# Optimization experiments

Measured on AMD Instinct MI355X. Metric: run time of the kernel, lower is better.

The kernel has to match this reference:

```python
import jax, jax.numpy as jnp
import numpy as np

K = 8            # hard-coded knn k
NS = 0.2         # LeakyReLU negative slope
EPS = 1e-6
LN_EPS = 1e-5
H = 6            # num_heads


def vn_lin(W, x):
    # VNLinear: linear over vector-channel dim (axis 1). x: (B, Cin, 3, ...)
    return jnp.einsum('oc,bc...->bo...', W, x)


def vn_leaky(x, W, U):
    # VNLinearLeakyReLU (no BN): feature map p, direction map d
    p = vn_lin(W, x)
    d = vn_lin(U, x)
    dot = jnp.sum(p * d, axis=2, keepdims=True)
    dsq = jnp.sum(d * d, axis=2, keepdims=True)
    neg = p - (dot / (dsq + EPS)) * d
    return NS * p + (1.0 - NS) * jnp.where(dot >= 0, p, neg)


def vn_layernorm(x, g, b):
    # LayerNorm on per-channel vector norms, rescale directions. x: (B,C,3,N)
    n = jnp.sqrt(jnp.sum(x * x, axis=2) + EPS)            # (B,C,N)
    mu = jnp.mean(n, axis=1, keepdims=True)
    var = jnp.var(n, axis=1, keepdims=True)
    nhat = (n - mu) / jnp.sqrt(var + LN_EPS)
    nnew = g[None, :, None] * nhat + b[None, :, None]
    return x * (nnew / n)[:, :, None, :]


def vn_attention(vn_x, Wq, Wk, Wv, Wo):
    # vn_x: (B, C, 3, N); VNLinear(C, 3C) projections, multi-head SDPA over N
    B, C, _, N = vn_x.shape
    def heads(W):
        t = vn_lin(W, vn_x)                               # (B, 3C, 3, N)
        t = t.reshape(B, H, 3 * C // H, 3, N)
        return t.transpose(0, 1, 4, 2, 3).reshape(B, H, N, -1)  # (B,H,N,9C/H)
    q, k, v = heads(Wq), heads(Wk), heads(Wv)
    scale = (3 * C // H) ** -0.5                          # head_dim = dim//H = 64
    attn = jax.nn.softmax(jnp.einsum('bhqd,bhkd->bhqk', q, k) * scale, axis=-1)
    o = jnp.einsum('bhqk,bhkd->bhqd', attn, v)            # (B,H,N,9C/H)
    o = o.transpose(0, 2, 1, 3).reshape(B, N, 3 * C, 3).transpose(0, 2, 3, 1)
    return vn_lin(Wo, o)                                  # (B, C, 3, N)


def vn_get_graph_feature(x, knn_index):
    # x: (B, C, 3, N); knn_index: flat (B*K*N,) into (B*N) rows
    B, C, _, N = x.shape
    xp = x.transpose(0, 3, 1, 2).reshape(B * N, C * 3)
    feat = xp[knn_index].reshape(B, K, N, C, 3)
    xc = x.transpose(0, 3, 1, 2).reshape(B, 1, N, C, 3)
    f = jnp.concatenate([feat - xc, jnp.broadcast_to(xc, (B, K, N, C, 3))], axis=3)
    return f.transpose(0, 3, 4, 2, 1)                     # (B, 2C, 3, N, K)


def setup_inputs() -> dict:
    key = jax.random.key(0)
    ks = jax.random.split(key, 20)
    B, N, C = 4, 2048, 128
    def w(k, o, i):
        return jax.random.normal(k, (o, i), jnp.float32) * (i ** -0.5)
    return {
        'x': jax.random.normal(ks[0], (B, N, 3 * C), jnp.float32),
        'knn_index': jax.random.randint(ks[1], (B * K * N,), 0, B * N),
        'g1': jnp.ones((C,), jnp.float32), 'b1': jnp.zeros((C,), jnp.float32),
        'g2': jnp.ones((C,), jnp.float32), 'b2': jnp.zeros((C,), jnp.float32),
        'Wq': w(ks[2], 3 * C, C), 'Wk': w(ks[3], 3 * C, C), 'Wv': w(ks[4], 3 * C, C),
        'Wo': w(ks[5], C, 3 * C),
        'W1': w(ks[6], C, 2 * C), 'U1': w(ks[7], C, 2 * C),   # conv1: 256->128
        'W2': w(ks[8], C, 2 * C),                               # conv2: 256->128
        'W3': w(ks[9], 2 * C, C), 'U3': w(ks[10], 2 * C, C),   # conv3: 128->256
        'W4': w(ks[11], C, 2 * C), 'U4': w(ks[12], C, 2 * C),  # conv4: 256->128
    }


def reference(x, knn_index, g1, b1, g2, b2, Wq, Wk, Wv, Wo, W1, U1, W2, W3, U3, W4, U4):
    B, N, D = x.shape
    C = D // 3
    vn_x = x.transpose(0, 2, 1).reshape(B, C, 3, N)
    norm_x = vn_layernorm(vn_x, g1, b1)
    x_1 = vn_attention(norm_x, Wq, Wk, Wv, Wo)            # (B,C,3,N)
    knn_f = vn_get_graph_feature(norm_x, knn_index)       # (B,2C,3,N,K)
    knn_f = vn_leaky(knn_f, W1, U1)                       # (B,C,3,N,K)
    knn_f = jnp.mean(knn_f, axis=-1)                      # mean_pool over k
    x_1 = jnp.concatenate([x_1, knn_f], axis=1)           # (B,2C,3,N)
    x_1 = vn_lin(W2, x_1)                                 # (B,C,3,N)
    vn_x = vn_x + x_1
    nx2 = vn_layernorm(vn_x, g2, b2)
    h = vn_leaky(nx2, W3, U3)                             # (B,2C,3,N)
    h = vn_leaky(h, W4, U4)                               # (B,C,3,N)
    vn_x = vn_x + h
    return vn_x.reshape(B, D, N).transpose(0, 2, 1)       # (B,N,384)
```

## Files before the change

### kernel.cpp

```cpp
#include <hip/hip_runtime.h>
#include <math.h>

#define NFIX 2048
#define HH 6
#define KNN 8
#define NSLOPE 0.2f
#define EPSF 1e-6f
#define LNEPSF 1e-5f
#define QSCALE 0.18033688011112042f
#define NSPLIT 2

typedef unsigned short ushort_t;
typedef unsigned int uint_t;
typedef __attribute__((ext_vector_type(8))) short bf16x8;
typedef __attribute__((ext_vector_type(4))) short bf16x4;
typedef __attribute__((ext_vector_type(8))) _Float16 f16x8;
typedef __attribute__((ext_vector_type(4))) _Float16 f16x4;
typedef __attribute__((ext_vector_type(16))) float f32x16;
typedef __attribute__((ext_vector_type(4))) float f32x4;

__device__ __forceinline__ ushort_t f2bf(float f) {
  union { float f; unsigned u; } v; v.f = f;
  unsigned r = v.u + 0x7fff + ((v.u >> 16) & 1);
  return (ushort_t)(r >> 16);
}
__device__ __forceinline__ float bf2f(ushort_t u) {
  union { uint_t u; float f; } v; v.u = ((uint_t)u) << 16; return v.f;
}
__device__ __forceinline__ uint_t pack2(float a, float b) {
  return (uint_t)f2bf(a) | ((uint_t)f2bf(b) << 16);
}
__device__ __forceinline__ ushort_t f2h_bits(float a) {
  union { _Float16 h; ushort_t s; } cv; cv.h = (_Float16)a; return cv.s;
}
__device__ __forceinline__ uint_t packh2(float a, float b) {
  union { _Float16 h; ushort_t s; } ha, hb;
  ha.h = (_Float16)a; hb.h = (_Float16)b;
  return (uint_t)ha.s | ((uint_t)hb.s << 16);
}

__device__ __forceinline__ void vnleaky3(const float* p, const float* dv, float* out) {
  float dot = p[0]*dv[0] + p[1]*dv[1] + p[2]*dv[2];
  float dsq = dv[0]*dv[0] + dv[1]*dv[1] + dv[2]*dv[2] + EPSF;
  float f = dot / dsq;
#pragma unroll
  for (int d = 0; d < 3; ++d) {
    float neg = p[d] - f * dv[d];
    out[d] = NSLOPE * p[d] + (1.f - NSLOPE) * ((dot >= 0.f) ? p[d] : neg);
  }
}

__global__ __launch_bounds__(256) void prep_ln1(
    const float* __restrict__ Wq, const float* __restrict__ Wk,
    const float* __restrict__ Wv, const float* __restrict__ Wo,
    const float* __restrict__ W1, const float* __restrict__ U1,
    const float* __restrict__ W2, const float* __restrict__ W3,
    const float* __restrict__ U3, const float* __restrict__ W4,
    const float* __restrict__ U4,
    ushort_t* __restrict__ Wall, _Float16* __restrict__ Af16,
    _Float16* __restrict__ W3h, _Float16* __restrict__ U3h,
    _Float16* __restrict__ W4h, _Float16* __restrict__ U4h,
    const float* __restrict__ xin, ushort_t* __restrict__ xbp,
    float* __restrict__ xdi, const float* __restrict__ g1,
    const float* __restrict__ b1) {
  __shared__ float red[8];
  int bi = blockIdx.x;
  if (bi >= 1600) {
    int t = threadIdx.x;
    int half = t >> 7, c = t & 127;
    int bn = (bi - 1600) * 2 + half;
    const float* row = xin + (size_t)bn * 384;
    float x0 = row[c*3+0], x1 = row[c*3+1], x2 = row[c*3+2];
    float nv = sqrtf(x0*x0 + x1*x1 + x2*x2 + EPSF);
    float s1 = nv, s2 = nv*nv;
#pragma unroll
    for (int off = 32; off >= 1; off >>= 1) {
      s1 += __shfl_down(s1, off);
      s2 += __shfl_down(s2, off);
    }
    int lane = t & 63, w = t >> 6;
    if (lane == 0) { red[w*2] = s1; red[w*2+1] = s2; }
    __syncthreads();
    int rb4 = (w >> 1) * 4;
    float tot1 = red[rb4] + red[rb4+2], tot2 = red[rb4+1] + red[rb4+3];
    float mu  = tot1 * (1.f/128.f);
    float var = tot2 * (1.f/128.f) - mu*mu;
    float rsig = rsqrtf(var + LNEPSF);
    float nnew = g1[c] * ((nv - mu) * rsig) + b1[c];
    float sc = nnew / nv;
    size_t rb = (size_t)bn * 384;
    xbp[rb + c]       = f2bf(x0*sc);
    xbp[rb + 128 + c] = f2bf(x1*sc);
    xbp[rb + 256 + c] = f2bf(x2*sc);
    xdi[rb + c]       = x0;
    xdi[rb + 128 + c] = x1;
    xdi[rb + 256 + c] = x2;
    return;
  }
  int idx = bi * 256 + threadIdx.x;
  if (idx < 212992) {
    int m = idx >> 7, c = idx & 127;
    float val;
    if (m < 384)       val = Wq[m*128 + c] * QSCALE;
    else if (m < 768)  val = Wk[(m-384)*128 + c];
    else if (m < 1152) val = Wv[(m-768)*128 + c];
    else {
      int j = m - 1152;
      if (j < 128)      val = W1[j*256 + c];
      else if (j < 256) val = U1[(j-128)*256 + c];
      else if (j < 384) { int o = j-256; val = W1[o*256 + 128 + c] - W1[o*256 + c]; }
      else              { int o = j-384; val = U1[o*256 + 128 + c] - U1[o*256 + c]; }
    }
    Wall[idx] = f2bf(val); return;
  }
  idx -= 212992;
  if (idx < 49152) {
    int c = idx / 384, j = idx % 384;
    float s = 0.f;
    for (int cp = 0; cp < 128; ++cp) s += W2[c*256 + cp] * Wo[cp*384 + j];
    Af16[(size_t)c*512 + j] = (_Float16)s; return;
  }
  idx -= 49152;
  if (idx < 16384) {
    int c2 = idx / 128, c = idx % 128;
    Af16[(size_t)c*512 + 384 + c2] = (_Float16)W2[c*256 + 128 + c2]; return;
  }
  idx -= 16384;
  if (idx < 32768) { W3h[idx] = (_Float16)W3[idx]; return; }
  idx -= 32768;
  if (idx < 32768) { U3h[idx] = (_Float16)U3[idx]; return; }
  idx -= 32768;
  if (idx < 32768) { W4h[idx] = (_Float16)W4[idx]; return; }
  idx -= 32768;
  if (idx < 32768) { U4h[idx] = (_Float16)U4[idx]; return; }
}

#define XT_PITCH 132
#define WT_PITCH 132
#define TR_PITCH 36
__global__ __launch_bounds__(256, 2) void qkv_conv1_mfma(
    const ushort_t* __restrict__ xb, const ushort_t* __restrict__ Wall,
    ushort_t* __restrict__ q, ushort_t* __restrict__ k, ushort_t* __restrict__ v,
    _Float16* __restrict__ YZh, _Float16* __restrict__ NBh) {
  __shared__ ushort_t xs[128*XT_PITCH];
  __shared__ ushort_t wt[2][32*WT_PITCH];
  __shared__ float tr[4][32*TR_PITCH];
  int nb = blockIdx.x % 192;
  int mq = blockIdx.x / 192;
  int n0 = nb * 128;
  int t = threadIdx.x;
  int w = t >> 6, lane = t & 63, ql = lane & 31, hl = lane >> 5;
  for (int idx = t; idx < 2048; idx += 256) {
    int n = idx >> 4, c16 = idx & 15;
    bf16x8 gv = *(const bf16x8*)&xb[(size_t)(n0 + n)*128 + c16*8];
    ushort_t* dst = &xs[n*XT_PITCH + c16*8];
    *(bf16x4*)dst = __builtin_shufflevector(gv, gv, 0, 1, 2, 3);
    *(bf16x4*)(dst+4) = __builtin_shufflevector(gv, gv, 4, 5, 6, 7);
  }
#pragma unroll
  for (int i = 0; i < 2; ++i) {
    int idx = i*256 + t;
    int mm = idx >> 4, c16 = idx & 15;
    bf16x8 gv = *(const bf16x8*)&Wall[(size_t)(mq*416 + mm)*128 + c16*8];
    ushort_t* dst = &wt[0][mm*WT_PITCH + c16*8];
    *(bf16x4*)dst = __builtin_shufflevector(gv, gv, 0, 1, 2, 3);
    *(bf16x4*)(dst+4) = __builtin_shufflevector(gv, gv, 4, 5, 6, 7);
  }
  __syncthreads();
  bf16x8 xf[8];
  {
    const ushort_t* xr = &xs[(w*32 + ql)*XT_PITCH + hl*8];
#pragma unroll
    for (int cs = 0; cs < 8; ++cs) {
      bf16x4 lo = *(const bf16x4*)(xr + cs*16);
      bf16x4 hi = *(const bf16x4*)(xr + cs*16 + 4);
      xf[cs] = __builtin_shufflevector(lo, hi, 0, 1, 2, 3, 4, 5, 6, 7);
    }
  }
  int ng = n0 + w*32 + ql;
  int pt = ng / 3;
  int d  = ng - 3*pt;
  float* trw = tr[w];
  int mm0 = t >> 4, c160 = t & 15;
  int mm1 = (t + 256) >> 4, c161 = t & 15;
  for (int mt = 0; mt < 13; ++mt) {
    int m0 = mq*416 + mt*32;
    int cur = mt & 1;
    bf16x8 wpre0, wpre1;
    if (mt < 12) {
      int m0n = m0 + 32;
      wpre0 = *(const bf16x8*)&Wall[(size_t)(m0n + mm0)*128 + c160*8];
      wpre1 = *(const bf16x8*)&Wall[(size_t)(m0n + mm1)*128 + c161*8];
    }
    f32x16 acc;
#pragma unroll
    for (int r = 0; r < 16; ++r) acc[r] = 0.f;
    const ushort_t* wr = &wt[cur][ql*WT_PITCH + hl*8];
#pragma unroll
    for (int cs = 0; cs < 8; ++cs) {
      bf16x4 lo = *(const bf16x4*)(wr + cs*16);
      bf16x4 hi = *(const bf16x4*)(wr + cs*16 + 4);
      bf16x8 af = __builtin_shufflevector(lo, hi, 0, 1, 2, 3, 4, 5, 6, 7);
      acc = __builtin_amdgcn_mfma_f32_32x32x16_bf16(af, xf[cs], acc, 0, 0, 0);
    }
#pragma unroll
    for (int r = 0; r < 16; ++r) {
      int mrow = (r&3) + 8*(r>>2) + 4*hl;
      trw[ql*TR_PITCH + mrow] = acc[r];
    }
    asm volatile("s_waitcnt lgkmcnt(0)" ::: "memory");
    float4 c0 = *(float4*)&trw[ql*TR_PITCH + hl*16 + 0];
    float4 c1 = *(float4*)&trw[ql*TR_PITCH + hl*16 + 4];
    float4 c2 = *(float4*)&trw[ql*TR_PITCH + hl*16 + 8];
    float4 c3 = *(float4*)&trw[ql*TR_PITCH + hl*16 + 12];
    asm volatile("s_waitcnt lgkmcnt(0)" ::: "memory");
    int mg = m0 + hl*16;
    if (m0 < 1152) {
      uint4 s0, s1;
      s0.x = pack2(c0.x, c0.y); s0.y = pack2(c0.z, c0.w);
      s0.z = pack2(c1.x, c1.y); s0.w = pack2(c1.z, c1.w);
      s1.x = pack2(c2.x, c2.y); s1.y = pack2(c2.z, c2.w);
      s1.z = pack2(c3.x, c3.y); s1.w = pack2(c3.z, c3.w);
      ushort_t* dst;
      if (m0 < 384)       dst = q + (size_t)pt*1152 + d*384 + mg;
      else if (m0 < 768)  dst = k + (size_t)pt*1152 + d*384 + (mg - 384);
      else                dst = v + (size_t)pt*1152 + d*384 + (mg - 768);
      *(uint4*)dst = s0;
      *(uint4*)(dst + 8) = s1;
    } else {
      int mat = mg - 1152;
      int sub = mat >> 7, o = mat & 127;
      _Float16* basep = (sub < 2) ? YZh : NBh;
      _Float16* dst = basep + (size_t)pt*768 + d*256 + (sub & 1)*128 + o;
      uint4 s0, s1;
      s0.x = packh2(c0.x, c0.y); s0.y = packh2(c0.z, c0.w);
      s0.z = packh2(c1.x, c1.y); s0.w = packh2(c1.z, c1.w);
      s1.x = packh2(c2.x, c2.y); s1.y = packh2(c2.z, c2.w);
      s1.z = packh2(c3.x, c3.y); s1.w = packh2(c3.z, c3.w);
      *(uint4*)dst = s0;
      *(uint4*)(dst + 8) = s1;
    }
    if (mt < 12) {
      int nxt = cur ^ 1;
      ushort_t* d0 = &wt[nxt][mm0*WT_PITCH + c160*8];
      *(bf16x4*)d0 = __builtin_shufflevector(wpre0, wpre0, 0, 1, 2, 3);
      *(bf16x4*)(d0+4) = __builtin_shufflevector(wpre0, wpre0, 4, 5, 6, 7);
      ushort_t* d1 = &wt[nxt][mm1*WT_PITCH + c161*8];
      *(bf16x4*)d1 = __builtin_shufflevector(wpre1, wpre1, 0, 1, 2, 3);
      *(bf16x4*)(d1+4) = __builtin_shufflevector(wpre1, wpre1, 4, 5, 6, 7);
    }
    __syncthreads();
  }
}

#define VT_LP 196
__global__ __launch_bounds__(256) void vtrans_kernel(const ushort_t* __restrict__ v,
    ushort_t* __restrict__ vT) {
  __shared__ ushort_t tl[64*VT_LP];
  int blk = blockIdx.x;
  int t = threadIdx.x;
  int bh = blk / 32, ptile = blk % 32;
  int b = bh / HH, h = bh % HH;
  int pt0 = ptile * 64;
#pragma unroll
  for (int i = 0; i < 6; ++i) {
    int u = i*256 + t;
    int p = u / 24, seg = u % 24;
    int d = seg >> 3, c8 = seg & 7;
    bf16x8 gv = *(const bf16x8*)&v[(size_t)(b*NFIX + pt0 + p)*1152 + d*384 + h*64 + c8*8];
    ushort_t* dst = &tl[p*VT_LP + d*64 + c8*8];
    *(bf16x4*)dst = __builtin_shufflevector(gv, gv, 0, 1, 2, 3);
    *(bf16x4*)(dst+4) = __builtin_shufflevector(gv, gv, 4, 5, 6, 7);
  }
  __syncthreads();
#pragma unroll
  for (int i = 0; i < 6; ++i) {
    int u = i*256 + t;
    int ch = u >> 3, pc = u & 7;
    int ol = ch / 3, dd = ch - 3*ol;
    int cloc = dd*64 + ol;
    ushort_t hv[8];
#pragma unroll
    for (int e = 0; e < 8; ++e)
      hv[e] = tl[(pc*8 + e)*VT_LP + cloc];
    uint4 o4;
    o4.x = (uint_t)hv[0] | ((uint_t)hv[1] << 16);
    o4.y = (uint_t)hv[2] | ((uint_t)hv[3] << 16);
    o4.z = (uint_t)hv[4] | ((uint_t)hv[5] << 16);
    o4.w = (uint_t)hv[6] | ((uint_t)hv[7] << 16);
    *(uint4*)&vT[((size_t)bh*192 + ch)*2048 + pt0 + pc*8] = o4;
  }
}

#define KT_P 196
#define VT_P 36
#define TW_P 195
__global__ __launch_bounds__(256, 2) void attn_kernel(const ushort_t* __restrict__ q,
    const ushort_t* __restrict__ k, const ushort_t* __restrict__ vT,
    ushort_t* __restrict__ opart, float* __restrict__ lpart,
    const _Float16* __restrict__ YZh, const _Float16* __restrict__ NBh,
    const int* __restrict__ knn_index, _Float16* __restrict__ kmf16) {
  __shared__ ushort_t kt[2][32*KT_P];
  __shared__ ushort_t vt[2][192*VT_P];
  __shared__ float alds[4][32];
  __shared__ int sidx[8][KNN];
  int blk = blockIdx.x;
  int t = threadIdx.x;
  if (blk >= 768) {
    int bnb = (blk - 768) * 8;
    int half = t >> 7, c = t & 127;
    if (t < 64) {
      int pi = t >> 3, kk = t & 7;
      int bn = bnb + pi;
      int b = bn / NFIX, n = bn % NFIX;
      sidx[pi][kk] = knn_index[(b*KNN + kk)*NFIX + n];
    }
    __syncthreads();
#pragma unroll
    for (int pi2 = 0; pi2 < 4; ++pi2) {
      int pi = half*4 + pi2;
      int bn = bnb + pi;
      float yb[3], zb[3];
#pragma unroll
      for (int d = 0; d < 3; ++d) {
        yb[d] = (float)NBh[(size_t)bn*768 + d*256 + c];
        zb[d] = (float)NBh[(size_t)bn*768 + d*256 + 128 + c];
      }
      float om[3] = {0.f, 0.f, 0.f};
#pragma unroll
      for (int kk = 0; kk < KNN; ++kk) {
        const _Float16* r = YZh + (size_t)sidx[pi][kk]*768;
        float p[3], dd[3];
#pragma unroll
        for (int d = 0; d < 3; ++d) {
          p[d]  = (float)r[d*256 + c] + yb[d];
          dd[d] = (float)r[d*256 + 128 + c] + zb[d];
        }
        float res[3];
        vnleaky3(p, dd, res);
        om[0] += res[0]; om[1] += res[1]; om[2] += res[2];
      }
#pragma unroll
      for (int d = 0; d < 3; ++d)
        kmf16[((size_t)bn*3 + d)*128 + c] = (_Float16)(om[d] * (1.f/KNN));
    }
    return;
  }
  int xcd = blk & 7, j = blk >> 3;
  int g = xcd*6 + (j >> 4);
  int qt = j & 15;
  int bh = g % 24;
  int split = g / 24;
  int b = bh / HH, h = bh % HH;
  int w = t >> 6, lane = t & 63, ql = lane & 31, hl = lane >> 5;
  int qrow0 = qt*128 + w*32;
  const ushort_t* qpb = q + (size_t)(b*NFIX + qrow0 + ql)*1152 + h*64;
  bf16x8 qf[12];
#pragma unroll
  for (int cs = 0; cs < 12; ++cs) {
    int red0 = cs*16 + hl*8;
    int dq = red0 >> 6, ml = red0 & 63;
    qf[cs] = *(const bf16x8*)(qpb + dq*384 + ml);
  }
  const ushort_t* ksrc[3]; int kdsto[3];
  const ushort_t* vsrc[3]; int vdsto[3];
#pragma unroll
  for (int j2 = 0; j2 < 3; ++j2) {
    int idx = t + j2*256;
    int kp = idx / 24, c16 = idx % 24;
    int red0 = c16*8;
    int dk = red0 >> 6, ml = red0 & 63;
    ksrc[j2] = k + (size_t)(b*NFIX + kp)*1152 + dk*384 + h*64 + ml;
    kdsto[j2] = kp*KT_P + c16*8;
    int ch = idx >> 2, c4 = idx & 3;
    vsrc[j2] = vT + ((size_t)bh*192 + ch)*2048 + c4*8;
    vdsto[j2] = ch*VT_P + c4*8;
  }
  f32x16 acc[6];
#pragma unroll
  for (int nt = 0; nt < 6; ++nt)
#pragma unroll
    for (int r = 0; r < 16; ++r) acc[nt][r] = 0.f;
  float lsum = 0.f;
  int koff0 = split * 1024;
  bf16x8 kpre[3], vpre[3];
#pragma unroll
  for (int j2 = 0; j2 < 3; ++j2) {
    kpre[j2] = *(const bf16x8*)(ksrc[j2] + (size_t)koff0*1152);
    vpre[j2] = *(const bf16x8*)(vsrc[j2] + koff0);
  }
#pragma unroll
  for (int j2 = 0; j2 < 3; ++j2) {
    ushort_t* kd = &kt[0][kdsto[j2]];
    *(bf16x4*)kd = __builtin_shufflevector(kpre[j2], kpre[j2], 0, 1, 2, 3);
    *(bf16x4*)(kd+4) = __builtin_shufflevector(kpre[j2], kpre[j2], 4, 5, 6, 7);
    ushort_t* vd = &vt[0][vdsto[j2]];
    *(bf16x4*)vd = __builtin_shufflevector(vpre[j2], vpre[j2], 0, 1, 2, 3);
    *(bf16x4*)(vd+4) = __builtin_shufflevector(vpre[j2], vpre[j2], 4, 5, 6, 7);
  }
  __syncthreads();
  for (int kb = 0; kb < 32; ++kb) {
    int cur = kb & 1;
    if (kb < 31) {
      int koff = koff0 + (kb+1)*32;
#pragma unroll
      for (int j2 = 0; j2 < 3; ++j2) {
        kpre[j2] = *(const bf16x8*)(ksrc[j2] + (size_t)koff*1152);
        vpre[j2] = *(const bf16x8*)(vsrc[j2] + koff);
      }
    }
    f32x16 sca, scb;
#pragma unroll
    for (int r = 0; r < 16; ++r) { sca[r] = 0.f; scb[r] = 0.f; }
    const ushort_t* ktc = kt[cur];
#pragma unroll
    for (int cs = 0; cs < 12; ++cs) {
      const ushort_t* kr = &ktc[ql*KT_P + cs*16 + hl*8];
      bf16x4 alo = *(const bf16x4*)kr;
      bf16x4 ahi = *(const bf16x4*)(kr + 4);
      bf16x8 af = __builtin_shufflevector(alo, ahi, 0, 1, 2, 3, 4, 5, 6, 7);
      if (cs & 1) scb = __builtin_amdgcn_mfma_f32_32x32x16_bf16(af, qf[cs], scb, 0, 0, 0);
      else        sca = __builtin_amdgcn_mfma_f32_32x32x16_bf16(af, qf[cs], sca, 0, 0, 0);
    }
    uint_t u[8], pex[8];
#pragma unroll
    for (int g2 = 0; g2 < 4; ++g2) {
      float p0 = __builtin_amdgcn_exp2f(sca[g2*4 + 0] + scb[g2*4 + 0]);
      float p1 = __builtin_amdgcn_exp2f(sca[g2*4 + 1] + scb[g2*4 + 1]);
      float p2 = __builtin_amdgcn_exp2f(sca[g2*4 + 2] + scb[g2*4 + 2]);
      float p3 = __builtin_amdgcn_exp2f(sca[g2*4 + 3] + scb[g2*4 + 3]);
      lsum += (p0 + p1) + (p2 + p3);
      u[2*g2]   = pack2(p0, p1);
      u[2*g2+1] = pack2(p2, p3);
    }
#pragma unroll
    for (int j2 = 0; j2 < 8; ++j2) pex[j2] = (uint_t)__shfl_xor((int)u[j2], 32);
    const ushort_t* vtc = vt[cur];
#pragma unroll
    for (int s = 0; s < 2; ++s) {
      uint4 au;
      au.x = hl ? pex[4*s+2] : u[4*s+0];
      au.y = hl ? pex[4*s+3] : u[4*s+1];
      au.z = hl ? u[4*s+2]   : pex[4*s+0];
      au.w = hl ? u[4*s+3]   : pex[4*s+1];
      union { uint4 ui; bf16x8 bv; } cvt; cvt.ui = au;
      bf16x8 pa = cvt.bv;
#pragma unroll
      for (int nt = 0; nt < 6; ++nt) {
        const ushort_t* vr = &vtc[(nt*32 + ql)*VT_P + s*16 + hl*8];
        bf16x4 vlo = *(const bf16x4*)vr;
        bf16x4 vhi = *(const bf16x4*)(vr + 4);
        bf16x8 vf = __builtin_shufflevector(vlo, vhi, 0, 1, 2, 3, 4, 5, 6, 7);
        acc[nt] = __builtin_amdgcn_mfma_f32_32x32x16_bf16(pa, vf, acc[nt], 0, 0, 0);
      }
    }
    if (kb < 31) {
      int nxt = cur ^ 1;
#pragma unroll
      for (int j2 = 0; j2 < 3; ++j2) {
        ushort_t* kd = &kt[nxt][kdsto[j2]];
        *(bf16x4*)kd = __builtin_shufflevector(kpre[j2], kpre[j2], 0, 1, 2, 3);
        *(bf16x4*)(kd+4) = __builtin_shufflevector(kpre[j2], kpre[j2], 4, 5, 6, 7);
        ushort_t* vd = &vt[nxt][vdsto[j2]];
        *(bf16x4*)vd = __builtin_shufflevector(vpre[j2], vpre[j2], 0, 1, 2, 3);
        *(bf16x4*)(vd+4) = __builtin_shufflevector(vpre[j2], vpre[j2], 4, 5, 6, 7);
      }
    }
    __syncthreads();
  }
  lsum += __shfl_xor(lsum, 32);
  if (lane < 32) {
    alds[w][ql] = 1.0f / lsum;
    lpart[(size_t)split*24*NFIX + (size_t)bh*NFIX + qrow0 + ql] = lsum;
  }
  asm volatile("s_waitcnt lgkmcnt(0)" ::: "memory");
  float lv[4][4];
#pragma unroll
  for (int g2 = 0; g2 < 4; ++g2) {
    f32x4 tv = *(const f32x4*)&alds[w][8*g2 + 4*hl];
#pragma unroll
    for (int rr = 0; rr < 4; ++rr) lv[g2][rr] = tv[rr];
  }
  ushort_t* tw = (w == 0) ? kt[0] : (w == 1) ? kt[1] : (w == 2) ? vt[0] : vt[1];
#pragma unroll
  for (int nt = 0; nt < 6; ++nt) {
    int ch = nt*32 + ql;
#pragma unroll
    for (int r = 0; r < 16; ++r) {
      int qrow = (r&3) + 8*(r>>2) + 4*hl;
      tw[qrow*TW_P + ch] = f2h_bits(acc[nt][r] * lv[r>>2][r&3]);
    }
  }
  asm volatile("s_waitcnt lgkmcnt(0)" ::: "memory");
  const size_t SS = (size_t)8192*1152;
  ushort_t* opb = opart + (size_t)split*SS;
  size_t nbase = (size_t)(b*NFIX + qrow0) * 3;
#pragma unroll
  for (int i = 0; i < 12; ++i) {
    int chunk = i*64 + lane;
    int nl = chunk >> 3, jc = chunk & 7;
    int qq = nl / 3, dd = nl - 3*qq;
    ushort_t hv[8];
#pragma unroll
    for (int e = 0; e < 8; ++e)
      hv[e] = tw[qq*TW_P + (jc*8 + e)*3 + dd];
    uint4 sv;
    sv.x = (uint_t)hv[0] | ((uint_t)hv[1] << 16);
    sv.y = (uint_t)hv[2] | ((uint_t)hv[3] << 16);
    sv.z = (uint_t)hv[4] | ((uint_t)hv[5] << 16);
    sv.w = (uint_t)hv[6] | ((uint_t)hv[7] << 16);
    *(uint4*)&opb[(nbase + nl)*384 + h*64 + jc*8] = sv;
  }
}

#define AP 68
#define XLP 132
#define X3P 132
#define HP4 260
#define TF4P 388
__global__ __launch_bounds__(768) void x1mid_c34(
    const float* __restrict__ xdi, const ushort_t* __restrict__ opart,
    const float* __restrict__ lpart, const _Float16* __restrict__ kmf16,
    const _Float16* __restrict__ Af16, const float* __restrict__ g2,
    const float* __restrict__ b2,
    const _Float16* __restrict__ W3h, const _Float16* __restrict__ U3h,
    const _Float16* __restrict__ W4h, const _Float16* __restrict__ U4h,
    float* __restrict__ out) {
  __shared__ __align__(16) char smem[50944];
  _Float16* As = (_Float16*)smem;
  _Float16* Bt = (_Float16*)(smem + 17408);
  float* wlsL  = (float*)(smem + 30464);
  float* X     = (float*)smem;
  float* stats = (float*)(smem + 50688);
  _Float16* Xs3 = (_Float16*)smem;
  _Float16* H   = (_Float16*)smem;
  float* trF    = (float*)smem;
  int blk = blockIdx.x;
  int n0 = blk * 96;
  int pt0 = blk * 32;
  int t = threadIdx.x;
  int w = t >> 6, lane = t & 63, ql = lane & 31, hl = lane >> 5;
  int nsub = w >> 2, mt2 = w & 3;
  if (t < 192) {
    int ptl = t / 6, h = t % 6;
    int ptg = pt0 + ptl;
    int b = ptg >> 11, n = ptg & 2047;
    size_t lidx = (size_t)(b*HH + h)*NFIX + n;
    float l[NSPLIT]; float tot = 0.f;
#pragma unroll
    for (int s = 0; s < NSPLIT; ++s) {
      l[s] = lpart[(size_t)s*24*NFIX + lidx];
      tot += l[s];
    }
    float rd = 1.f / tot;
    float* wp = &wlsL[(ptl*6 + h)*NSPLIT];
#pragma unroll
    for (int s = 0; s < NSPLIT; ++s) wp[s] = l[s]*rd;
  }
  f32x16 acc;
#pragma unroll
  for (int r = 0; r < 16; ++r) acc[r] = 0.f;
  const size_t SS = (size_t)8192*1152;
  __syncthreads();
  for (int p = 0; p < 8; ++p) {
    for (int u = t; u < 1024; u += 768) {
      int m = u >> 3, kc = u & 7;
      f16x4 a0 = *(const f16x4*)&Af16[(size_t)m*512 + p*64 + kc*8];
      f16x4 a1 = *(const f16x4*)&Af16[(size_t)m*512 + p*64 + kc*8 + 4];
      _Float16* dst = &As[m*AP + kc*8];
      *(f16x4*)dst = a0;
      *(f16x4*)(dst+4) = a1;
    }
    {
      int n_l = t >> 3, jc = t & 7;
      int n_g = n0 + n_l;
      _Float16* dst = &Bt[n_l*AP + jc*8];
      if (p < 6) {
        int pt_l = n_l / 3;
        const float* wp = &wlsL[(pt_l*6 + p)*NSPLIT];
        float facc[8];
#pragma unroll
        for (int e = 0; e < 8; ++e) facc[e] = 0.f;
#pragma unroll
        for (int s = 0; s < NSPLIT; ++s) {
          const ushort_t* src = opart + s*SS + (size_t)n_g*384 + p*64 + jc*8;
          uint4 ra = *(const uint4*)src;
          const _Float16* ua = (const _Float16*)&ra;
          float wsc = wp[s];
#pragma unroll
          for (int e = 0; e < 8; ++e)
            facc[e] += wsc * (float)ua[e];
        }
        _Float16 hv[8];
#pragma unroll
        for (int e = 0; e < 8; ++e) hv[e] = (_Float16)facc[e];
        *(f16x4*)dst = *(f16x4*)&hv[0];
        *(f16x4*)(dst+4) = *(f16x4*)&hv[4];
      } else {
        const _Float16* src = kmf16 + (size_t)n_g*128 + (p-6)*64 + jc*8;
        f16x4 v0 = *(const f16x4*)src;
        f16x4 v1 = *(const f16x4*)(src + 4);
        *(f16x4*)dst = v0; *(f16x4*)(dst+4) = v1;
      }
    }
    __syncthreads();
#pragma unroll
    for (int cs = 0; cs < 4; ++cs) {
      int kloc = cs*16 + hl*8;
      f16x4 b0 = *(const f16x4*)&Bt[(nsub*32 + ql)*AP + kloc];
      f16x4 b1 = *(const f16x4*)&Bt[(nsub*32 + ql)*AP + kloc + 4];
      f16x8 bf = __builtin_shufflevector(b0, b1, 0, 1, 2, 3, 4, 5, 6, 7);
      int mrow = mt2*32 + ql;
      f16x4 a0 = *(const f16x4*)&As[mrow*AP + kloc];
      f16x4 a1 = *(const f16x4*)&As[mrow*AP + kloc + 4];
      f16x8 af = __builtin_shufflevector(a0, a1, 0, 1, 2, 3, 4, 5, 6, 7);
      acc = __builtin_amdgcn_mfma_f32_32x32x16_f16(af, bf, acc, 0, 0, 0);
    }
    __syncthreads();
  }
  {
    int cbase = mt2*32 + 4*hl;
    float* xrow = &X[(nsub*32 + ql)*XLP];
#pragma unroll
    for (int r = 0; r < 16; ++r) {
      int col = cbase + (r&3) + 8*(r>>2);
      xrow[col] = acc[r];
    }
  }
  __syncthreads();
#pragma unroll
  for (int i = 0; i < 2; ++i) {
    int u = i*768 + t;
    int row = u >> 4, c0 = (u & 15) * 8;
    float* xp = &X[row*XLP + c0];
    const float* xd = xdi + (size_t)(n0 + row)*128 + c0;
    float4 a0 = *(float4*)xp, a1 = *(float4*)(xp + 4);
    float4 d0 = *(const float4*)xd, d1 = *(const float4*)(xd + 4);
    a0.x += d0.x; a0.y += d0.y; a0.z += d0.z; a0.w += d0.w;
    a1.x += d1.x; a1.y += d1.y; a1.z += d1.z; a1.w += d1.w;
    *(float4*)xp = a0; *(float4*)(xp + 4) = a1;
  }
  __syncthreads();
  float rs[16];
#pragma unroll
  for (int i = 0; i < 4; ++i) {
    int u = i*768 + t;
    int row = u / 96, c4 = u % 96;
#pragma unroll
    for (int e = 0; e < 4; ++e) {
      int col = c4*4 + e;
      int o = col / 3, dd = col - 3*o;
      rs[i*4 + e] = X[(3*row + dd)*XLP + o];
    }
  }
  for (int pi = w; pi < 32; pi += 12) {
    int c = lane;
    float a0 = X[(pi*3+0)*XLP + c], a1 = X[(pi*3+1)*XLP + c], a2 = X[(pi*3+2)*XLP + c];
    float e0 = X[(pi*3+0)*XLP + c + 64], e1 = X[(pi*3+1)*XLP + c + 64], e2 = X[(pi*3+2)*XLP + c + 64];
    float nva = sqrtf(a0*a0 + a1*a1 + a2*a2 + EPSF);
    float nvb = sqrtf(e0*e0 + e1*e1 + e2*e2 + EPSF);
    float s1 = nva + nvb;
    float s2 = nva*nva + nvb*nvb;
#pragma unroll
    for (int off = 32; off >= 1; off >>= 1) {
      s1 += __shfl_down(s1, off);
      s2 += __shfl_down(s2, off);
    }
    if (lane == 0) {
      float mu = s1 * (1.f/128.f);
      float var = s2 * (1.f/128.f) - mu*mu;
      stats[pi*2]   = mu;
      stats[pi*2+1] = rsqrtf(var + LNEPSF);
    }
  }
  __syncthreads();
  uint4 svr[2]; int rowr[2], c0r[2];
#pragma unroll
  for (int i = 0; i < 2; ++i) {
    int u = i*768 + t;
    int row = u >> 4, c0 = (u & 15) * 8;
    int pt_l = row / 3;
    float mu = stats[pt_l*2], rsig = stats[pt_l*2+1];
    const float* r0 = &X[(pt_l*3 + 0)*XLP + c0];
    const float* r1 = &X[(pt_l*3 + 1)*XLP + c0];
    const float* r2 = &X[(pt_l*3 + 2)*XLP + c0];
    const float* rd = &X[row*XLP + c0];
    float xv[8];
#pragma unroll
    for (int e = 0; e < 8; ++e) {
      float x0 = r0[e], x1 = r1[e], x2 = r2[e];
      float nv = sqrtf(x0*x0 + x1*x1 + x2*x2 + EPSF);
      float nnew = g2[c0 + e] * ((nv - mu) * rsig) + b2[c0 + e];
      xv[e] = rd[e] * (nnew / nv);
    }
    uint4 sv;
    sv.x = packh2(xv[0], xv[1]); sv.y = packh2(xv[2], xv[3]);
    sv.z = packh2(xv[4], xv[5]); sv.w = packh2(xv[6], xv[7]);
    svr[i] = sv; rowr[i] = row; c0r[i] = c0;
  }
  __syncthreads();
#pragma unroll
  for (int i = 0; i < 2; ++i) {
    int row = rowr[i];
    int d = row % 3, p = row / 3;
    _Float16* dst = &Xs3[(d*32 + p)*X3P + c0r[i]];
    uint2 lo; lo.x = svr[i].x; lo.y = svr[i].y;
    uint2 hi; hi.x = svr[i].z; hi.y = svr[i].w;
    *(uint2*)dst = lo;
    *(uint2*)(dst + 4) = hi;
  }
  __syncthreads();
  f32x16 accP[3], accD[3];
  int ot3 = w*32;
  if (w < 8) {
#pragma unroll
    for (int d = 0; d < 3; ++d)
#pragma unroll
      for (int r = 0; r < 16; ++r) { accP[d][r] = 0.f; accD[d][r] = 0.f; }
    const _Float16* Wp = W3h + (size_t)(ot3 + ql)*128 + hl*8;
    const _Float16* Up = U3h + (size_t)(ot3 + ql)*128 + hl*8;
#pragma unroll
    for (int cs = 0; cs < 8; ++cs) {
      f16x8 wf = *(const f16x8*)(Wp + cs*16);
      f16x8 uf = *(const f16x8*)(Up + cs*16);
#pragma unroll
      for (int d = 0; d < 3; ++d) {
        const _Float16* xr = &Xs3[(d*32 + ql)*X3P + cs*16 + hl*8];
        f16x4 lo = *(const f16x4*)xr;
        f16x4 hi = *(const f16x4*)(xr + 4);
        f16x8 xf = __builtin_shufflevector(lo, hi, 0, 1, 2, 3, 4, 5, 6, 7);
        accP[d] = __builtin_amdgcn_mfma_f32_32x32x16_f16(wf, xf, accP[d], 0, 0, 0);
        accD[d] = __builtin_amdgcn_mfma_f32_32x32x16_f16(uf, xf, accD[d], 0, 0, 0);
      }
    }
  }
  __syncthreads();
  if (w < 8) {
#pragma unroll
    for (int r = 0; r < 16; ++r) {
      int olr = (r&3) + 8*(r>>2) + 4*hl;
      float p3[3], d3[3], res[3];
#pragma unroll
      for (int d = 0; d < 3; ++d) { p3[d] = accP[d][r]; d3[d] = accD[d][r]; }
      vnleaky3(p3, d3, res);
#pragma unroll
      for (int d = 0; d < 3; ++d)
        H[(d*32 + ql)*HP4 + ot3 + olr] = (_Float16)res[d];
    }
  }
  __syncthreads();
  int ph = w >> 2;
  int ot4 = (w & 3) * 32;
  int nl = lane & 15, kq = lane >> 4;
  f32x4 acc4P[2][3], acc4D[2][3];
  if (w < 8) {
#pragma unroll
    for (int mt = 0; mt < 2; ++mt)
#pragma unroll
      for (int d = 0; d < 3; ++d)
#pragma unroll
        for (int r = 0; r < 4; ++r) { acc4P[mt][d][r] = 0.f; acc4D[mt][d][r] = 0.f; }
    const _Float16* Wb = W4h + (size_t)ot4*256;
    const _Float16* Ub = U4h + (size_t)ot4*256;
#pragma unroll
    for (int cs = 0; cs < 8; ++cs) {
      int kof = cs*32 + kq*8;
      f16x8 xf[3];
#pragma unroll
      for (int d = 0; d < 3; ++d) {
        const _Float16* xr = &H[(d*32 + ph*16 + nl)*HP4 + kof];
        f16x4 lo = *(const f16x4*)xr;
        f16x4 hi = *(const f16x4*)(xr + 4);
        xf[d] = __builtin_shufflevector(lo, hi, 0, 1, 2, 3, 4, 5, 6, 7);
      }
#pragma unroll
      for (int mt = 0; mt < 2; ++mt) {
        f16x8 wf = *(const f16x8*)(Wb + (size_t)(mt*16 + nl)*256 + kof);
        f16x8 uf = *(const f16x8*)(Ub + (size_t)(mt*16 + nl)*256 + kof);
#pragma unroll
        for (int d = 0; d < 3; ++d) {
          acc4P[mt][d] = __builtin_amdgcn_mfma_f32_16x16x32_f16(wf, xf[d], acc4P[mt][d], 0, 0, 0);
          acc4D[mt][d] = __builtin_amdgcn_mfma_f32_16x16x32_f16(uf, xf[d], acc4D[mt][d], 0, 0, 0);
        }
      }
    }
  }
  __syncthreads();
  if (w < 8) {
#pragma unroll
    for (int mt = 0; mt < 2; ++mt)
#pragma unroll
      for (int r = 0; r < 4; ++r) {
        int o = ot4 + mt*16 + kq*4 + r;
        int p_l = ph*16 + nl;
        float p3[3], d3[3], res[3];
#pragma unroll
        for (int d = 0; d < 3; ++d) { p3[d] = acc4P[mt][d][r]; d3[d] = acc4D[mt][d][r]; }
        vnleaky3(p3, d3, res);
#pragma unroll
        for (int d = 0; d < 3; ++d) trF[p_l*TF4P + o*3 + d] = res[d];
      }
  }
  __syncthreads();
#pragma unroll
  for (int i = 0; i < 4; ++i) {
    int u = i*768 + t;
    int row = u / 96, c4 = u % 96;
    float4 vv = *(float4*)&trF[row*TF4P + c4*4];
    int bn = pt0 + row;
    float4 ov;
    ov.x = vv.x + rs[i*4 + 0];
    ov.y = vv.y + rs[i*4 + 1];
    ov.z = vv.z + rs[i*4 + 2];
    ov.w = vv.w + rs[i*4 + 3];
    *(float4*)&out[(size_t)bn*384 + c4*4] = ov;
  }
}

extern "C" void kernel_launch(void* const* d_in, const int* in_sizes, int n_in,
                              void* d_out, int out_size, void* d_ws, size_t ws_size,
                              hipStream_t stream) {
  const float* x   = (const float*)d_in[0];
  const int* knn   = (const int*)d_in[1];
  const float* g1  = (const float*)d_in[2];
  const float* b1  = (const float*)d_in[3];
  const float* g2  = (const float*)d_in[4];
  const float* b2  = (const float*)d_in[5];
  const float* Wq  = (const float*)d_in[6];
  const float* Wk  = (const float*)d_in[7];
  const float* Wv  = (const float*)d_in[8];
  const float* Wo  = (const float*)d_in[9];
  const float* W1  = (const float*)d_in[10];
  const float* U1  = (const float*)d_in[11];
  const float* W2  = (const float*)d_in[12];
  const float* W3  = (const float*)d_in[13];
  const float* U3  = (const float*)d_in[14];
  const float* W4  = (const float*)d_in[15];
  const float* U4  = (const float*)d_in[16];
  float* out = (float*)d_out;
  (void)n_in; (void)out_size; (void)ws_size;

  const size_t BN = (size_t)in_sizes[0] / 384;

  float* ws    = (float*)d_ws;
  float* xdi   = ws;
  float* xmid  = xdi + BN*384;
  _Float16* kmf16 = (_Float16*)(xmid + BN*384);
  ushort_t* xbp = (ushort_t*)(kmf16 + BN*384);
  ushort_t* qb = xbp + BN*384;
  ushort_t* kb = qb + BN*1152;
  ushort_t* vb = kb + BN*1152;
  ushort_t* vT = vb + BN*1152;
  ushort_t* Wall = vT + BN*1152;
  _Float16* Af16 = (_Float16*)(Wall + 212992);
  _Float16* W3h = Af16 + 65536;
  _Float16* U3h = W3h + 32768;
  _Float16* W4h = U3h + 32768;
  _Float16* U4h = W4h + 32768;
  ushort_t* opart = (ushort_t*)(U4h + 32768);
  float* lpart = (float*)(opart + 4*BN*1152);
  _Float16* YZh = (_Float16*)(opart + 2*BN*1152);
  _Float16* NBh = YZh + BN*768;

  prep_ln1<<<1600 + 4096, 256, 0, stream>>>(Wq, Wk, Wv, Wo, W1, U1, W2, W3, U3, W4, U4,
                                            Wall, Af16, W3h, U3h, W4h, U4h,
                                            x, xbp, xdi, g1, b1);
  qkv_conv1_mfma<<<192*4, 256, 0, stream>>>(xbp, Wall, qb, kb, vb, YZh, NBh);
  vtrans_kernel<<<768, 256, 0, stream>>>(vb, vT);
  attn_kernel<<<16*24*NSPLIT + 1024, 256, 0, stream>>>(qb, kb, vT, opart, lpart,
                                                       YZh, NBh, knn, kmf16);
  x1mid_c34<<<256, 768, 0, stream>>>(xdi, opart, lpart, kmf16, Af16, g2, b2,
                                     W3h, U3h, W4h, U4h, out);
}
```

Before: 283.0 us.

## Move conv1 projection GEMM from QKV kernel into V-transpose kernel launch

The fused projection kernel used to compute Q/K/V plus the conv1 (YZ/NB) outputs across 4 row groups of 416 rows each. It now computes only Q/K/V across 3 groups of 384 rows. The 512 conv1 rows are done by 192 extra blocks appended to the V-transpose launch, which now has a shared-memory union for both roles. This balances per-block work and fills the otherwise lightweight transpose launch with GEMM work. The cost is that xb and the conv1 weights are loaded again in the second kernel, and the transpose kernel now needs more shared memory, which can lower its occupancy.

Result: no change. 285.6 us (+0.9%).

```diff
diff --git a/kernel.cpp b/kernel.cpp
--- a/kernel.cpp
+++ b/kernel.cpp
@@ -138,10 +138,9 @@
 #define XT_PITCH 132
 #define WT_PITCH 132
 #define TR_PITCH 36
-__global__ __launch_bounds__(256, 2) void qkv_conv1_mfma(
+__global__ __launch_bounds__(256, 2) void qkv_mfma(
     const ushort_t* __restrict__ xb, const ushort_t* __restrict__ Wall,
-    ushort_t* __restrict__ q, ushort_t* __restrict__ k, ushort_t* __restrict__ v,
-    _Float16* __restrict__ YZh, _Float16* __restrict__ NBh) {
+    ushort_t* __restrict__ q, ushort_t* __restrict__ k, ushort_t* __restrict__ v) {
   __shared__ ushort_t xs[128*XT_PITCH];
   __shared__ ushort_t wt[2][32*WT_PITCH];
   __shared__ float tr[4][32*TR_PITCH];
@@ -161,7 +160,7 @@
   for (int i = 0; i < 2; ++i) {
     int idx = i*256 + t;
     int mm = idx >> 4, c16 = idx & 15;
-    bf16x8 gv = *(const bf16x8*)&Wall[(size_t)(mq*416 + mm)*128 + c16*8];
+    bf16x8 gv = *(const bf16x8*)&Wall[(size_t)(mq*384 + mm)*128 + c16*8];
     ushort_t* dst = &wt[0][mm*WT_PITCH + c16*8];
     *(bf16x4*)dst = __builtin_shufflevector(gv, gv, 0, 1, 2, 3);
     *(bf16x4*)(dst+4) = __builtin_shufflevector(gv, gv, 4, 5, 6, 7);
@@ -183,11 +182,11 @@
   float* trw = tr[w];
   int mm0 = t >> 4, c160 = t & 15;
   int mm1 = (t + 256) >> 4, c161 = t & 15;
-  for (int mt = 0; mt < 13; ++mt) {
-    int m0 = mq*416 + mt*32;
+  for (int mt = 0; mt < 12; ++mt) {
+    int m0 = mq*384 + mt*32;
     int cur = mt & 1;
     bf16x8 wpre0, wpre1;
-    if (mt < 12) {
+    if (mt < 11) {
       int m0n = m0 + 32;
       wpre0 = *(const bf16x8*)&Wall[(size_t)(m0n + mm0)*128 + c160*8];
       wpre1 = *(const bf16x8*)&Wall[(size_t)(m0n + mm1)*128 + c161*8];
@@ -215,7 +214,7 @@
     float4 c3 = *(float4*)&trw[ql*TR_PITCH + hl*16 + 12];
     asm volatile("s_waitcnt lgkmcnt(0)" ::: "memory");
     int mg = m0 + hl*16;
-    if (m0 < 1152) {
+    {
       uint4 s0, s1;
       s0.x = pack2(c0.x, c0.y); s0.y = pack2(c0.z, c0.w);
       s0.z = pack2(c1.x, c1.y); s0.w = pack2(c1.z, c1.w);
@@ -227,7 +226,135 @@
       else                dst = v + (size_t)pt*1152 + d*384 + (mg - 768);
       *(uint4*)dst = s0;
       *(uint4*)(dst + 8) = s1;
-    } else {
+    }
+    if (mt < 11) {
+      int nxt = cur ^ 1;
+      ushort_t* d0 = &wt[nxt][mm0*WT_PITCH + c160*8];
+      *(bf16x4*)d0 = __builtin_shufflevector(wpre0, wpre0, 0, 1, 2, 3);
+      *(bf16x4*)(d0+4) = __builtin_shufflevector(wpre0, wpre0, 4, 5, 6, 7);
+      ushort_t* d1 = &wt[nxt][mm1*WT_PITCH + c161*8];
+      *(bf16x4*)d1 = __builtin_shufflevector(wpre1, wpre1, 0, 1, 2, 3);
+      *(bf16x4*)(d1+4) = __builtin_shufflevector(wpre1, wpre1, 4, 5, 6, 7);
+    }
+    __syncthreads();
+  }
+}
+
+#define VT_LP 196
+__global__ __launch_bounds__(256, 2) void vtrans_conv1(const ushort_t* __restrict__ v,
+    ushort_t* __restrict__ vT, const ushort_t* __restrict__ xb,
+    const ushort_t* __restrict__ Wall,
+    _Float16* __restrict__ YZh, _Float16* __restrict__ NBh) {
+  __shared__ __align__(16) char smem[69120];
+  int blk = blockIdx.x;
+  int t = threadIdx.x;
+  if (blk < 768) {
+    ushort_t* tl = (ushort_t*)smem;
+    int bh = blk / 32, ptile = blk % 32;
+    int b = bh / HH, h = bh % HH;
+    int pt0 = ptile * 64;
+#pragma unroll
+    for (int i = 0; i < 6; ++i) {
+      int u = i*256 + t;
+      int p = u / 24, seg = u % 24;
+      int d = seg >> 3, c8 = seg & 7;
+      bf16x8 gv = *(const bf16x8*)&v[(size_t)(b*NFIX + pt0 + p)*1152 + d*384 + h*64 + c8*8];
+      ushort_t* dst = &tl[p*VT_LP + d*64 + c8*8];
+      *(bf16x4*)dst = __builtin_shufflevector(gv, gv, 0, 1, 2, 3);
+      *(bf16x4*)(dst+4) = __builtin_shufflevector(gv, gv, 4, 5, 6, 7);
+    }
+    __syncthreads();
+#pragma unroll
+    for (int i = 0; i < 6; ++i) {
+      int u = i*256 + t;
+      int ch = u >> 3, pc = u & 7;
+      int ol = ch / 3, dd = ch - 3*ol;
+      int cloc = dd*64 + ol;
+      ushort_t hv[8];
+#pragma unroll
+      for (int e = 0; e < 8; ++e)
+        hv[e] = tl[(pc*8 + e)*VT_LP + cloc];
+      uint4 o4;
+      o4.x = (uint_t)hv[0] | ((uint_t)hv[1] << 16);
+      o4.y = (uint_t)hv[2] | ((uint_t)hv[3] << 16);
+      o4.z = (uint_t)hv[4] | ((uint_t)hv[5] << 16);
+      o4.w = (uint_t)hv[6] | ((uint_t)hv[7] << 16);
+      *(uint4*)&vT[((size_t)bh*192 + ch)*2048 + pt0 + pc*8] = o4;
+    }
+    return;
+  }
+  ushort_t* xs = (ushort_t*)smem;
+  ushort_t* wtb = (ushort_t*)(smem + 33792);
+  float* trb = (float*)(smem + 50688);
+  int nb = blk - 768;
+  int n0 = nb * 128;
+  int w = t >> 6, lane = t & 63, ql = lane & 31, hl = lane >> 5;
+  for (int idx = t; idx < 2048; idx += 256) {
+    int n = idx >> 4, c16 = idx & 15;
+    bf16x8 gv = *(const bf16x8*)&xb[(size_t)(n0 + n)*128 + c16*8];
+    ushort_t* dst = &xs[n*XT_PITCH + c16*8];
+    *(bf16x4*)dst = __builtin_shufflevector(gv, gv, 0, 1, 2, 3);
+    *(bf16x4*)(dst+4) = __builtin_shufflevector(gv, gv, 4, 5, 6, 7);
+  }
+#pragma unroll
+  for (int i = 0; i < 2; ++i) {
+    int idx = i*256 + t;
+    int mm = idx >> 4, c16 = idx & 15;
+    bf16x8 gv = *(const bf16x8*)&Wall[(size_t)(1152 + mm)*128 + c16*8];
+    ushort_t* dst = &wtb[mm*WT_PITCH + c16*8];
+    *(bf16x4*)dst = __builtin_shufflevector(gv, gv, 0, 1, 2, 3);
+    *(bf16x4*)(dst+4) = __builtin_shufflevector(gv, gv, 4, 5, 6, 7);
+  }
+  __syncthreads();
+  bf16x8 xf[8];
+  {
+    const ushort_t* xr = &xs[(w*32 + ql)*XT_PITCH + hl*8];
+#pragma unroll
+    for (int cs = 0; cs < 8; ++cs) {
+      bf16x4 lo = *(const bf16x4*)(xr + cs*16);
+      bf16x4 hi = *(const bf16x4*)(xr + cs*16 + 4);
+      xf[cs] = __builtin_shufflevector(lo, hi, 0, 1, 2, 3, 4, 5, 6, 7);
+    }
+  }
+  int ng = n0 + w*32 + ql;
+  int pt = ng / 3;
+  int d  = ng - 3*pt;
+  float* trw = trb + w*32*TR_PITCH;
+  int mm0 = t >> 4, c160 = t & 15;
+  int mm1 = (t + 256) >> 4, c161 = t & 15;
+  for (int mt = 0; mt < 16; ++mt) {
+    int m0 = 1152 + mt*32;
+    int cur = mt & 1;
+    bf16x8 wpre0, wpre1;
+    if (mt < 15) {
+      int m0n = m0 + 32;
+      wpre0 = *(const bf16x8*)&Wall[(size_t)(m0n + mm0)*128 + c160*8];
+      wpre1 = *(const bf16x8*)&Wall[(size_t)(m0n + mm1)*128 + c161*8];
+    }
+    f32x16 acc;
+#pragma unroll
+    for (int r = 0; r < 16; ++r) acc[r] = 0.f;
+    const ushort_t* wr = &wtb[cur*32*WT_PITCH + ql*WT_PITCH + hl*8];
+#pragma unroll
+    for (int cs = 0; cs < 8; ++cs) {
+      bf16x4 lo = *(const bf16x4*)(wr + cs*16);
+      bf16x4 hi = *(const bf16x4*)(wr + cs*16 + 4);
+      bf16x8 af = __builtin_shufflevector(lo, hi, 0, 1, 2, 3, 4, 5, 6, 7);
+      acc = __builtin_amdgcn_mfma_f32_32x32x16_bf16(af, xf[cs], acc, 0, 0, 0);
+    }
+#pragma unroll
+    for (int r = 0; r < 16; ++r) {
+      int mrow = (r&3) + 8*(r>>2) + 4*hl;
+      trw[ql*TR_PITCH + mrow] = acc[r];
+    }
+    asm volatile("s_waitcnt lgkmcnt(0)" ::: "memory");
+    float4 c0 = *(float4*)&trw[ql*TR_PITCH + hl*16 + 0];
+    float4 c1 = *(float4*)&trw[ql*TR_PITCH + hl*16 + 4];
+    float4 c2 = *(float4*)&trw[ql*TR_PITCH + hl*16 + 8];
+    float4 c3 = *(float4*)&trw[ql*TR_PITCH + hl*16 + 12];
+    asm volatile("s_waitcnt lgkmcnt(0)" ::: "memory");
+    int mg = m0 + hl*16;
+    {
       int mat = mg - 1152;
       int sub = mat >> 7, o = mat & 127;
       _Float16* basep = (sub < 2) ? YZh : NBh;
@@ -240,55 +367,16 @@
       *(uint4*)dst = s0;
       *(uint4*)(dst + 8) = s1;
     }
-    if (mt < 12) {
+    if (mt < 15) {
       int nxt = cur ^ 1;
-      ushort_t* d0 = &wt[nxt][mm0*WT_PITCH + c160*8];
+      ushort_t* d0 = &wtb[nxt*32*WT_PITCH + mm0*WT_PITCH + c160*8];
       *(bf16x4*)d0 = __builtin_shufflevector(wpre0, wpre0, 0, 1, 2, 3);
       *(bf16x4*)(d0+4) = __builtin_shufflevector(wpre0, wpre0, 4, 5, 6, 7);
-      ushort_t* d1 = &wt[nxt][mm1*WT_PITCH + c161*8];
+      ushort_t* d1 = &wtb[nxt*32*WT_PITCH + mm1*WT_PITCH + c161*8];
       *(bf16x4*)d1 = __builtin_shufflevector(wpre1, wpre1, 0, 1, 2, 3);
       *(bf16x4*)(d1+4) = __builtin_shufflevector(wpre1, wpre1, 4, 5, 6, 7);
     }
     __syncthreads();
-  }
-}
-
-#define VT_LP 196
-__global__ __launch_bounds__(256) void vtrans_kernel(const ushort_t* __restrict__ v,
-    ushort_t* __restrict__ vT) {
-  __shared__ ushort_t tl[64*VT_LP];
-  int blk = blockIdx.x;
-  int t = threadIdx.x;
-  int bh = blk / 32, ptile = blk % 32;
-  int b = bh / HH, h = bh % HH;
-  int pt0 = ptile * 64;
-#pragma unroll
-  for (int i = 0; i < 6; ++i) {
-    int u = i*256 + t;
-    int p = u / 24, seg = u % 24;
-    int d = seg >> 3, c8 = seg & 7;
-    bf16x8 gv = *(const bf16x8*)&v[(size_t)(b*NFIX + pt0 + p)*1152 + d*384 + h*64 + c8*8];
-    ushort_t* dst = &tl[p*VT_LP + d*64 + c8*8];
-    *(bf16x4*)dst = __builtin_shufflevector(gv, gv, 0, 1, 2, 3);
-    *(bf16x4*)(dst+4) = __builtin_shufflevector(gv, gv, 4, 5, 6, 7);
-  }
-  __syncthreads();
-#pragma unroll
-  for (int i = 0; i < 6; ++i) {
-    int u = i*256 + t;
-    int ch = u >> 3, pc = u & 7;
-    int ol = ch / 3, dd = ch - 3*ol;
-    int cloc = dd*64 + ol;
-    ushort_t hv[8];
-#pragma unroll
-    for (int e = 0; e < 8; ++e)
-      hv[e] = tl[(pc*8 + e)*VT_LP + cloc];
-    uint4 o4;
-    o4.x = (uint_t)hv[0] | ((uint_t)hv[1] << 16);
-    o4.y = (uint_t)hv[2] | ((uint_t)hv[3] << 16);
-    o4.z = (uint_t)hv[4] | ((uint_t)hv[5] << 16);
-    o4.w = (uint_t)hv[6] | ((uint_t)hv[7] << 16);
-    *(uint4*)&vT[((size_t)bh*192 + ch)*2048 + pt0 + pc*8] = o4;
   }
 }
 
@@ -865,8 +953,8 @@
   prep_ln1<<<1600 + 4096, 256, 0, stream>>>(Wq, Wk, Wv, Wo, W1, U1, W2, W3, U3, W4, U4,
                                             Wall, Af16, W3h, U3h, W4h, U4h,
                                             x, xbp, xdi, g1, b1);
-  qkv_conv1_mfma<<<192*4, 256, 0, stream>>>(xbp, Wall, qb, kb, vb, YZh, NBh);
-  vtrans_kernel<<<768, 256, 0, stream>>>(vb, vT);
+  qkv_mfma<<<192*3, 256, 0, stream>>>(xbp, Wall, qb, kb, vb);
+  vtrans_conv1<<<768 + 192, 256, 0, stream>>>(vb, vT, xbp, Wall, YZh, NBh);
   attn_kernel<<<16*24*NSPLIT + 1024, 256, 0, stream>>>(qb, kb, vT, opart, lpart,
                                                        YZh, NBh, knn, kmf16);
   x1mid_c34<<<256, 768, 0, stream>>>(xdi, opart, lpart, kmf16, Af16, g2, b2,
```
